# Optimization experiments

Measured on AMD Instinct MI355X. Metric: run time of the kernel, lower is better.

Reference implementation:

```python
import jax, jax.numpy as jnp
from jax import lax
import numpy as np

PATCH_H = 8
PATCH_W = 8


def setup_inputs() -> dict:
    key = jax.random.key(0)
    k1, k2 = jax.random.split(key)
    x = jax.random.normal(k1, (2, 1024, 256, 256), dtype=jnp.float32)
    # Conv1d weight [C_out, C_in, k], bias=False
    conv_w = jax.random.normal(k2, (1024, 1024, 3), dtype=jnp.float32) * 0.02
    return {"x": x, "conv_w": conv_w}


def reference(x, conv_w):
    B, C, H, W = x.shape
    hf, wf = H // PATCH_H, W // PATCH_W
    P = hf * wf
    # Patch average pool: mean over each (PATCH_H, PATCH_W) tile -> [B, C, hf, wf]
    xp = x.reshape(B, C, hf, PATCH_H, wf, PATCH_W)
    y = xp.mean(axis=(3, 5)).reshape(B, C, P)
    # Conv1d over the patch axis (SAME padding, no bias), then sigmoid gate
    g = lax.conv_general_dilated(
        y, conv_w, window_strides=(1,), padding="SAME",
        dimension_numbers=("NCH", "OIH", "NCH"))
    g = jax.nn.sigmoid(g).reshape(B, C, hf, wf)
    # Broadcast gate back over each patch and multiply
    out = xp * g[:, :, :, None, :, None]
    return out.reshape(B, C, H, W)
```

## Files before the change

### kernel.cpp

```cpp
#include <hip/hip_runtime.h>
#include <hip/hip_bf16.h>

#define HH 256
#define WW 256
#define CCH 1024
#define PP 1024

using f32x4 = __attribute__((ext_vector_type(4))) float;
using short8 = __attribute__((ext_vector_type(8))) short;

__device__ __forceinline__ void pool_body(const float* __restrict__ xb,
                                          float* __restrict__ yb, int c, int t) {
    int wid  = t >> 6;
    int lane = t & 63;
    const float* xp = xb + (size_t)c * (HH * WW) + lane * 4;
    float* yp = yb + (size_t)c * PP;
#pragma unroll
    for (int s = 0; s < 8; ++s) {
        int ph = wid + s * 4;
        const float* slab = xp + (size_t)ph * 8 * WW;
        float acc = 0.f;
#pragma unroll
        for (int r = 0; r < 8; ++r) {
            f32x4 v = *(const f32x4*)(slab + (size_t)r * WW);
            acc += v.x + v.y + v.z + v.w;
        }
        acc += __shfl_xor(acc, 1);
        if ((lane & 1) == 0)
            yp[ph * 32 + (lane >> 1)] = acc * (1.f / 64.f);
    }
}

__device__ __forceinline__ void apply_body(const float* __restrict__ xb,
                                           const float* __restrict__ gateb,
                                           float* __restrict__ outb,
                                           float* __restrict__ g,
                                           int c, int t) {
    const float* xp = xb   + (size_t)c * (HH * WW);
    float*       op = outb + (size_t)c * (HH * WW);
    ((f32x4*)g)[t] = ((const f32x4*)(gateb + (size_t)c * PP))[t];
    __syncthreads();
    int col4 = t & 63;
    int r    = t >> 6;
    int pc   = col4 >> 1;
#pragma unroll 4
    for (int it = 0; it < 64; ++it) {
        int row = it * 4 + r;
        float gg = g[(row >> 3) * 32 + pc];
        size_t off = (size_t)row * 64 + col4;
        f32x4 v = *((const f32x4*)xp + off);
        v *= gg;
        __builtin_nontemporal_store(v, (f32x4*)op + off);
    }
}

__global__ __launch_bounds__(256) void pool0_wconv_kernel(
        const float* __restrict__ x, const float* __restrict__ w,
        float* __restrict__ y, __hip_bfloat16* __restrict__ wT,
        __hip_bfloat16* __restrict__ yT) {
    int bid = blockIdx.x, t = threadIdx.x;
    if (bid < 1024) {
        pool_body(x, y, bid, t);
    } else {
        int base = (bid - 1024) * 256 + t;
#pragma unroll
        for (int it = 0; it < 16; ++it) {
            int idx = it * (1 << 16) + base;
            const float* p = w + (size_t)idx * 3;
            wT[idx]               = __float2bfloat16(p[0]);
            wT[(1u << 20) + idx]  = __float2bfloat16(p[1]);
            wT[(2u << 20) + idx]  = __float2bfloat16(p[2]);
        }
        if (base < 2 * CCH) {
            int bb = base >> 10, cc = base & 1023;
            __hip_bfloat16 z = __float2bfloat16(0.f);
            __hip_bfloat16* basep = yT + (size_t)bb * (PP + 2) * CCH;
            basep[cc] = z;
            basep[(size_t)(PP + 1) * CCH + cc] = z;
        }
    }
}

__global__ __launch_bounds__(256) void apply0_pool1_kernel(
        const float* __restrict__ x, const float* __restrict__ gate,
        float* __restrict__ out, float* __restrict__ y) {
    __shared__ __align__(16) float g[PP];
    int bid = blockIdx.x, t = threadIdx.x;
    if (bid < 1024) {
        apply_body(x, gate, out, g, 1023 - bid, t);
    } else {
        const float* x1 = x + (size_t)CCH * HH * WW;
        float*       y1 = y + (size_t)CCH * PP;
        pool_body(x1, y1, bid - 1024, t);
    }
}

__global__ __launch_bounds__(256) void apply_kernel(const float* __restrict__ xb,
                                                    const float* __restrict__ gateb,
                                                    float* __restrict__ outb) {
    __shared__ __align__(16) float g[PP];
    apply_body(xb, gateb, outb, g, 1023 - blockIdx.x, threadIdx.x);
}

__global__ __launch_bounds__(256) void transpose_kernel(const float* __restrict__ yb,
                                                        __hip_bfloat16* __restrict__ yTb) {
    int c0 = blockIdx.x * 32;
    int p0 = blockIdx.y * 32;
    __shared__ float tile[32][33];
    int tx = threadIdx.x, ty = threadIdx.y;
#pragma unroll
    for (int rr = 0; rr < 4; ++rr)
        tile[ty + rr * 8][tx] = yb[(size_t)(c0 + ty + rr * 8) * PP + p0 + tx];
    __syncthreads();
#pragma unroll
    for (int rr = 0; rr < 4; ++rr)
        yTb[(size_t)(1 + p0 + ty + rr * 8) * CCH + c0 + tx] =
            __float2bfloat16(tile[tx][ty + rr * 8]);
}

__global__ __launch_bounds__(256) void conv_gemm_kernel(
        const __hip_bfloat16* __restrict__ wT,
        const __hip_bfloat16* __restrict__ yTb,
        float* __restrict__ gateb) {
    int lane = threadIdx.x & 63;
    int wid  = threadIdx.x >> 6;
    int l15 = lane & 15, lhi = lane >> 4;
    int co_base = blockIdx.x * 64 + wid * 16;
    int p_base  = blockIdx.y * 32;
    f32x4 acc[2] = {};
#pragma unroll
    for (int tap = 0; tap < 3; ++tap) {
        const __hip_bfloat16* Ap = wT + (size_t)tap * (1u << 20)
                                 + (size_t)(co_base + l15) * CCH + lhi * 8;
        const __hip_bfloat16* Bp = yTb + (size_t)(p_base + l15 + tap) * CCH + lhi * 8;
        for (int ci0 = 0; ci0 < CCH; ci0 += 32) {
            short8 a0 = *(const short8*)(Ap + ci0);
            short8 b0 = *(const short8*)(Bp + ci0);
            short8 b1 = *(const short8*)(Bp + ci0 + 16 * CCH);
            acc[0] = __builtin_amdgcn_mfma_f32_16x16x32_bf16(a0, b0, acc[0], 0, 0, 0);
            acc[1] = __builtin_amdgcn_mfma_f32_16x16x32_bf16(a0, b1, acc[1], 0, 0, 0);
        }
    }
#pragma unroll
    for (int j16 = 0; j16 < 2; ++j16) {
        int col  = p_base + j16 * 16 + l15;
        int row0 = co_base + lhi * 4;
#pragma unroll
        for (int r = 0; r < 4; ++r)
            gateb[(size_t)(row0 + r) * PP + col] = 1.f / (1.f + __expf(-acc[j16][r]));
    }
}

extern "C" void kernel_launch(void* const* d_in, const int* in_sizes, int n_in,
                              void* d_out, int out_size, void* d_ws, size_t ws_size,
                              hipStream_t stream) {
    const float* x = (const float*)d_in[0];
    const float* w = (const float*)d_in[1];
    float* out = (float*)d_out;

    char* ws = (char*)d_ws;
    float*          y    = (float*)(ws);
    __hip_bfloat16* yT   = (__hip_bfloat16*)(ws + 8388608);
    __hip_bfloat16* wT   = (__hip_bfloat16*)(ws + 12591104);
    float*          gate = (float*)(ws + 18882560);

    const float* x1    = x    + (size_t)CCH * HH * WW;
    float*       y1    = y    + (size_t)CCH * PP;
    __hip_bfloat16* yT1 = yT  + (size_t)(PP + 2) * CCH;
    float*       gate1 = gate + (size_t)CCH * PP;
    float*       out1  = out  + (size_t)CCH * HH * WW;

    hipLaunchKernelGGL(pool0_wconv_kernel, dim3(1280), dim3(256), 0, stream,
                       x, w, y, wT, yT);
    hipLaunchKernelGGL(transpose_kernel, dim3(32, 32), dim3(32, 8), 0, stream, y, yT);
    hipLaunchKernelGGL(conv_gemm_kernel, dim3(16, 32), dim3(256), 0, stream, wT, yT, gate);
    hipLaunchKernelGGL(apply0_pool1_kernel, dim3(2048), dim3(256), 0, stream,
                       x, gate, out, y);
    hipLaunchKernelGGL(transpose_kernel, dim3(32, 32), dim3(32, 8), 0, stream, y1, yT1);
    hipLaunchKernelGGL(conv_gemm_kernel, dim3(16, 32), dim3(256), 0, stream, wT, yT1, gate1);
    hipLaunchKernelGGL(apply_kernel, dim3(1024), dim3(256), 0, stream, x1, gate1, out1);
}
```

Before: 414.7 us.

## Pool directly into transposed bf16 and co-schedule GEMMs with pool/apply stages

The pooling stage now writes its output straight into the transposed bf16 layout through a shared-memory tile, which removes the separate fp32 intermediate and both transpose kernels. The pipeline is regrouped into four launches: batch 0's conv GEMM runs alongside batch 1's pooling, batch 1's GEMM runs alongside batch 0's apply, and batch 1's apply runs last. Loads of x now use nontemporal hints. The aim is fewer launches and fewer intermediate round-trips, with the small GEMMs hidden behind bandwidth-bound stages. The trade-off is that each pool block now reads 32 channels at a strided slab, which changes the access pattern, and the GEMM blocks share the GPU with the streaming blocks.

```diff
diff --git a/kernel.cpp b/kernel.cpp
--- a/kernel.cpp
+++ b/kernel.cpp
@@ -9,124 +9,49 @@
 using f32x4 = __attribute__((ext_vector_type(4))) float;
 using short8 = __attribute__((ext_vector_type(8))) short;
 
-__device__ __forceinline__ void pool_body(const float* __restrict__ xb,
-                                          float* __restrict__ yb, int c, int t) {
-    int wid  = t >> 6;
-    int lane = t & 63;
-    const float* xp = xb + (size_t)c * (HH * WW) + lane * 4;
-    float* yp = yb + (size_t)c * PP;
-#pragma unroll
-    for (int s = 0; s < 8; ++s) {
-        int ph = wid + s * 4;
-        const float* slab = xp + (size_t)ph * 8 * WW;
+__device__ __forceinline__ void pool_direct_body(const float* __restrict__ xb,
+                                                 __hip_bfloat16* __restrict__ yTb,
+                                                 int job, int t) {
+    __shared__ float lds[32][33];
+    int ph = job >> 5, c0 = (job & 31) * 32;
+    int wid = t >> 6, lane = t & 63;
+#pragma unroll 2
+    for (int i = 0; i < 8; ++i) {
+        int cl = wid * 8 + i;
+        const float* base = xb + (size_t)(c0 + cl) * (HH * WW)
+                          + (size_t)ph * 8 * WW + lane * 4;
         float acc = 0.f;
 #pragma unroll
         for (int r = 0; r < 8; ++r) {
-            f32x4 v = *(const f32x4*)(slab + (size_t)r * WW);
+            f32x4 v = __builtin_nontemporal_load((const f32x4*)(base + r * WW));
             acc += v.x + v.y + v.z + v.w;
         }
         acc += __shfl_xor(acc, 1);
         if ((lane & 1) == 0)
-            yp[ph * 32 + (lane >> 1)] = acc * (1.f / 64.f);
+            lds[lane >> 1][cl] = acc * (1.f / 64.f);
+    }
+    __syncthreads();
+    if (t < 128) {
+        int row = t >> 2, q = t & 3;
+        short8 s;
+#pragma unroll
+        for (int j = 0; j < 8; ++j) {
+            __hip_bfloat16 h = __float2bfloat16(lds[row][q * 8 + j]);
+            s[j] = (short)reinterpret_cast<unsigned short&>(h);
+        }
+        *(short8*)(yTb + (size_t)(1 + ph * 32 + row) * CCH + c0 + q * 8) = s;
     }
 }
 
-__device__ __forceinline__ void apply_body(const float* __restrict__ xb,
-                                           const float* __restrict__ gateb,
-                                           float* __restrict__ outb,
-                                           float* __restrict__ g,
-                                           int c, int t) {
-    const float* xp = xb   + (size_t)c * (HH * WW);
-    float*       op = outb + (size_t)c * (HH * WW);
-    ((f32x4*)g)[t] = ((const f32x4*)(gateb + (size_t)c * PP))[t];
-    __syncthreads();
-    int col4 = t & 63;
-    int r    = t >> 6;
-    int pc   = col4 >> 1;
-#pragma unroll 4
-    for (int it = 0; it < 64; ++it) {
-        int row = it * 4 + r;
-        float gg = g[(row >> 3) * 32 + pc];
-        size_t off = (size_t)row * 64 + col4;
-        f32x4 v = *((const f32x4*)xp + off);
-        v *= gg;
-        __builtin_nontemporal_store(v, (f32x4*)op + off);
-    }
-}
-
-__global__ __launch_bounds__(256) void pool0_wconv_kernel(
-        const float* __restrict__ x, const float* __restrict__ w,
-        float* __restrict__ y, __hip_bfloat16* __restrict__ wT,
-        __hip_bfloat16* __restrict__ yT) {
-    int bid = blockIdx.x, t = threadIdx.x;
-    if (bid < 1024) {
-        pool_body(x, y, bid, t);
-    } else {
-        int base = (bid - 1024) * 256 + t;
-#pragma unroll
-        for (int it = 0; it < 16; ++it) {
-            int idx = it * (1 << 16) + base;
-            const float* p = w + (size_t)idx * 3;
-            wT[idx]               = __float2bfloat16(p[0]);
-            wT[(1u << 20) + idx]  = __float2bfloat16(p[1]);
-            wT[(2u << 20) + idx]  = __float2bfloat16(p[2]);
-        }
-        if (base < 2 * CCH) {
-            int bb = base >> 10, cc = base & 1023;
-            __hip_bfloat16 z = __float2bfloat16(0.f);
-            __hip_bfloat16* basep = yT + (size_t)bb * (PP + 2) * CCH;
-            basep[cc] = z;
-            basep[(size_t)(PP + 1) * CCH + cc] = z;
-        }
-    }
-}
-
-__global__ __launch_bounds__(256) void apply0_pool1_kernel(
-        const float* __restrict__ x, const float* __restrict__ gate,
-        float* __restrict__ out, float* __restrict__ y) {
-    __shared__ __align__(16) float g[PP];
-    int bid = blockIdx.x, t = threadIdx.x;
-    if (bid < 1024) {
-        apply_body(x, gate, out, g, 1023 - bid, t);
-    } else {
-        const float* x1 = x + (size_t)CCH * HH * WW;
-        float*       y1 = y + (size_t)CCH * PP;
-        pool_body(x1, y1, bid - 1024, t);
-    }
-}
-
-__global__ __launch_bounds__(256) void apply_kernel(const float* __restrict__ xb,
-                                                    const float* __restrict__ gateb,
-                                                    float* __restrict__ outb) {
-    __shared__ __align__(16) float g[PP];
-    apply_body(xb, gateb, outb, g, 1023 - blockIdx.x, threadIdx.x);
-}
-
-__global__ __launch_bounds__(256) void transpose_kernel(const float* __restrict__ yb,
-                                                        __hip_bfloat16* __restrict__ yTb) {
-    int c0 = blockIdx.x * 32;
-    int p0 = blockIdx.y * 32;
-    __shared__ float tile[32][33];
-    int tx = threadIdx.x, ty = threadIdx.y;
-#pragma unroll
-    for (int rr = 0; rr < 4; ++rr)
-        tile[ty + rr * 8][tx] = yb[(size_t)(c0 + ty + rr * 8) * PP + p0 + tx];
-    __syncthreads();
-#pragma unroll
-    for (int rr = 0; rr < 4; ++rr)
-        yTb[(size_t)(1 + p0 + ty + rr * 8) * CCH + c0 + tx] =
-            __float2bfloat16(tile[tx][ty + rr * 8]);
-}
-
-__global__ __launch_bounds__(256) void conv_gemm_kernel(
-        const __hip_bfloat16* __restrict__ wT,
-        const __hip_bfloat16* __restrict__ yTb,
-        float* __restrict__ gateb) {
-    int lane = threadIdx.x & 63;
-    int wid  = threadIdx.x >> 6;
+__device__ __forceinline__ void gemm_body(const __hip_bfloat16* __restrict__ wT,
+                                          const __hip_bfloat16* __restrict__ yTb,
+                                          float* __restrict__ gateb,
+                                          int job, int tid) {
+    int lane = tid & 63;
+    int wid  = tid >> 6;
     int l15 = lane & 15, lhi = lane >> 4;
-    int co_base = blockIdx.x * 64 + wid * 16;
-    int p_base  = blockIdx.y * 32;
+    int co_base = (job & 15) * 64 + wid * 16;
+    int p_base  = (job >> 4) * 32;
     f32x4 acc[2] = {};
 #pragma unroll
     for (int tap = 0; tap < 3; ++tap) {
@@ -151,6 +76,91 @@
     }
 }
 
+__device__ __forceinline__ void apply_body(const float* __restrict__ xb,
+                                           const float* __restrict__ gateb,
+                                           float* __restrict__ outb,
+                                           int c, int t) {
+    __shared__ __align__(16) float g[PP];
+    const float* xp = xb   + (size_t)c * (HH * WW);
+    float*       op = outb + (size_t)c * (HH * WW);
+    ((f32x4*)g)[t] = ((const f32x4*)(gateb + (size_t)c * PP))[t];
+    __syncthreads();
+    int col4 = t & 63;
+    int r    = t >> 6;
+    int pc   = col4 >> 1;
+#pragma unroll 4
+    for (int it = 0; it < 64; ++it) {
+        int row = it * 4 + r;
+        float gg = g[(row >> 3) * 32 + pc];
+        size_t off = (size_t)row * 64 + col4;
+        f32x4 v = __builtin_nontemporal_load((const f32x4*)xp + off);
+        v *= gg;
+        __builtin_nontemporal_store(v, (f32x4*)op + off);
+    }
+}
+
+__global__ __launch_bounds__(256) void pool0_wconv_kernel(
+        const float* __restrict__ x, const float* __restrict__ w,
+        __hip_bfloat16* __restrict__ yT, __hip_bfloat16* __restrict__ wT) {
+    int bid = blockIdx.x, t = threadIdx.x;
+    if (bid < 1024) {
+        pool_direct_body(x, yT, bid, t);
+    } else {
+        int base = (bid - 1024) * 256 + t;
+#pragma unroll
+        for (int it = 0; it < 16; ++it) {
+            int idx = it * (1 << 16) + base;
+            const float* p = w + (size_t)idx * 3;
+            wT[idx]               = __float2bfloat16(p[0]);
+            wT[(1u << 20) + idx]  = __float2bfloat16(p[1]);
+            wT[(2u << 20) + idx]  = __float2bfloat16(p[2]);
+        }
+        if (base < 2 * CCH) {
+            int bb = base >> 10, cc = base & 1023;
+            __hip_bfloat16 z = __float2bfloat16(0.f);
+            __hip_bfloat16* basep = yT + (size_t)bb * (PP + 2) * CCH;
+            basep[cc] = z;
+            basep[(size_t)(PP + 1) * CCH + cc] = z;
+        }
+    }
+}
+
+__global__ __launch_bounds__(256) void gemm0_pool1_kernel(
+        const float* __restrict__ x, const __hip_bfloat16* __restrict__ wT,
+        __hip_bfloat16* __restrict__ yT, float* __restrict__ gate) {
+    int bid = blockIdx.x, t = threadIdx.x;
+    if (bid < 512) {
+        gemm_body(wT, yT, gate, bid, t);
+    } else {
+        const float* x1 = x + (size_t)CCH * HH * WW;
+        __hip_bfloat16* yT1 = yT + (size_t)(PP + 2) * CCH;
+        pool_direct_body(x1, yT1, bid - 512, t);
+    }
+}
+
+__global__ __launch_bounds__(256) void gemm1_apply0_kernel(
+        const float* __restrict__ x, const __hip_bfloat16* __restrict__ wT,
+        const __hip_bfloat16* __restrict__ yT, float* __restrict__ gate,
+        float* __restrict__ out) {
+    int bid = blockIdx.x, t = threadIdx.x;
+    if (bid < 512) {
+        const __hip_bfloat16* yT1 = yT + (size_t)(PP + 2) * CCH;
+        float* gate1 = gate + (size_t)CCH * PP;
+        gemm_body(wT, yT1, gate1, bid, t);
+    } else {
+        apply_body(x, gate, out, 1023 - (bid - 512), t);
+    }
+}
+
+__global__ __launch_bounds__(256) void apply1_kernel(
+        const float* __restrict__ x, const float* __restrict__ gate,
+        float* __restrict__ out) {
+    const float* x1    = x    + (size_t)CCH * HH * WW;
+    const float* gate1 = gate + (size_t)CCH * PP;
+    float*       out1  = out  + (size_t)CCH * HH * WW;
+    apply_body(x1, gate1, out1, 1023 - blockIdx.x, threadIdx.x);
+}
+
 extern "C" void kernel_launch(void* const* d_in, const int* in_sizes, int n_in,
                               void* d_out, int out_size, void* d_ws, size_t ws_size,
                               hipStream_t stream) {
@@ -159,24 +169,16 @@
     float* out = (float*)d_out;
 
     char* ws = (char*)d_ws;
-    float*          y    = (float*)(ws);
-    __hip_bfloat16* yT   = (__hip_bfloat16*)(ws + 8388608);
-    __hip_bfloat16* wT   = (__hip_bfloat16*)(ws + 12591104);
-    float*          gate = (float*)(ws + 18882560);
-
-    const float* x1    = x    + (size_t)CCH * HH * WW;
-    float*       y1    = y    + (size_t)CCH * PP;
-    __hip_bfloat16* yT1 = yT  + (size_t)(PP + 2) * CCH;
-    float*       gate1 = gate + (size_t)CCH * PP;
-    float*       out1  = out  + (size_t)CCH * HH * WW;
+    __hip_bfloat16* yT   = (__hip_bfloat16*)(ws);
+    __hip_bfloat16* wT   = (__hip_bfloat16*)(ws + 4202496);
+    float*          gate = (float*)(ws + 10493952);
 
     hipLaunchKernelGGL(pool0_wconv_kernel, dim3(1280), dim3(256), 0, stream,
-                       x, w, y, wT, yT);
-    hipLaunchKernelGGL(transpose_kernel, dim3(32, 32), dim3(32, 8), 0, stream, y, yT);
-    hipLaunchKernelGGL(conv_gemm_kernel, dim3(16, 32), dim3(256), 0, stream, wT, yT, gate);
-    hipLaunchKernelGGL(apply0_pool1_kernel, dim3(2048), dim3(256), 0, stream,
-                       x, gate, out, y);
-    hipLaunchKernelGGL(transpose_kernel, dim3(32, 32), dim3(32, 8), 0, stream, y1, yT1);
-    hipLaunchKernelGGL(conv_gemm_kernel, dim3(16, 32), dim3(256), 0, stream, wT, yT1, gate1);
-    hipLaunchKernelGGL(apply_kernel, dim3(1024), dim3(256), 0, stream, x1, gate1, out1);
+                       x, w, yT, wT);
+    hipLaunchKernelGGL(gemm0_pool1_kernel, dim3(1536), dim3(256), 0, stream,
+                       x, wT, yT, gate);
+    hipLaunchKernelGGL(gemm1_apply0_kernel, dim3(1536), dim3(256), 0, stream,
+                       x, wT, yT, gate, out);
+    hipLaunchKernelGGL(apply1_kernel, dim3(1024), dim3(256), 0, stream,
+                       x, gate, out);
 }
```

Result: faster. 404.4 us (-2.5%).
